# Performance work log

Hardware: AMD Instinct MI355X
Metric: run time of the kernel (lower is better)

The kernel has to match this reference:

```python
import jax, jax.numpy as jnp
import numpy as np

N = 40000      # nodes
E = 640000     # edges
R = 4          # relations (n_edge_features)
F = 128        # n_node_features
H = 128        # n_hidden
NB = 2         # num_convolution_blocks
G = 64         # graphs in batch
OUT = 10       # n_output
MAXDEG = 10    # PyG MFConv default max_degree


def setup_inputs() -> dict:
    key = jax.random.key(0)
    ks = jax.random.split(key, 20)
    s = 0.05
    return {
        "x": jax.random.normal(ks[0], (N, F), dtype=jnp.float32),
        "edge_index": jax.random.randint(ks[1], (2, E), 0, N, dtype=jnp.int32),
        "edge_attr": jax.random.randint(ks[2], (E,), 0, R, dtype=jnp.int32),
        "batch_idx": jnp.sort(jax.random.randint(ks[3], (N,), 0, G, dtype=jnp.int32)),
        # node embedding Linear(F -> H)
        "W0": jax.random.normal(ks[4], (F, H), dtype=jnp.float32) * s,
        "b0": jnp.zeros((H,), dtype=jnp.float32),
        # per-block RGCNConv params (stacked over blocks)
        "rgcn_Wrel": jax.random.normal(ks[5], (NB, R, H, H), dtype=jnp.float32) * s,
        "rgcn_Wroot": jax.random.normal(ks[6], (NB, H, H), dtype=jnp.float32) * s,
        "rgcn_b": jnp.zeros((NB, H), dtype=jnp.float32),
        # per-block MFConv params: lins_l (bias) and lins_r (no bias), one per degree 0..MAXDEG
        "mf_Wl": jax.random.normal(ks[7], (NB, MAXDEG + 1, H, H), dtype=jnp.float32) * s,
        "mf_bl": jnp.zeros((NB, MAXDEG + 1, H), dtype=jnp.float32),
        "mf_Wr": jax.random.normal(ks[8], (NB, MAXDEG + 1, H, H), dtype=jnp.float32) * s,
        # after-pool MLP
        "W1": jax.random.normal(ks[9], (H, H), dtype=jnp.float32) * s,
        "b1": jnp.zeros((H,), dtype=jnp.float32),
        "W2": jax.random.normal(ks[10], (H, OUT), dtype=jnp.float32) * s,
        "b2": jnp.zeros((OUT,), dtype=jnp.float32),
    }


def _rgcn(h, Wrel, Wroot, b, src, dst, etype):
    # PyG RGCNConv: per-relation mean of neighbor features, then relation GEMM, plus root + bias
    n = h.shape[0]
    idx = dst * R + etype                                   # fused (node, relation) segment id
    msg = h[src]                                            # [E, H] gather
    sums = jax.ops.segment_sum(msg, idx, num_segments=n * R).reshape(n, R, -1)
    cnt = jax.ops.segment_sum(jnp.ones((msg.shape[0],), h.dtype), idx,
                              num_segments=n * R).reshape(n, R, 1)
    mean = jnp.where(cnt > 0, sums / jnp.maximum(cnt, 1.0), 0.0)
    return jnp.einsum('nrh,rho->no', mean, Wrel) + h @ Wroot + b


def _mfconv(h, Wl, bl, Wr, src, dst, deg):
    # PyG MFConv: sum-aggregate neighbors, then degree-specific lin_l(agg) + lin_r(x)
    n = h.shape[0]
    agg = jax.ops.segment_sum(h[src], dst, num_segments=n)  # [N, H]
    out = jnp.zeros((n, Wl.shape[-1]), h.dtype)
    for d in range(MAXDEG + 1):                             # small fixed loop over degree buckets
        m = (deg == d).astype(h.dtype)[:, None]
        out = out + m * (agg @ Wl[d] + bl[d] + h @ Wr[d])
    return out


def reference(x, edge_index, edge_attr, batch_idx,
              W0, b0, rgcn_Wrel, rgcn_Wroot, rgcn_b,
              mf_Wl, mf_bl, mf_Wr, W1, b1, W2, b2):
    src, dst = edge_index[0], edge_index[1]
    etype = edge_attr
    n = x.shape[0]
    # node degree at targets (all relations), clamped to MAXDEG (PyG MFConv)
    deg = jnp.clip(jax.ops.segment_sum(jnp.ones((src.shape[0],), jnp.int32), dst,
                                       num_segments=n), 0, MAXDEG)
    h = x @ W0 + b0
    for blk in range(NB):
        h = jax.nn.relu(h)
        h = _rgcn(h, rgcn_Wrel[blk], rgcn_Wroot[blk], rgcn_b[blk], src, dst, etype)
        h = jax.nn.relu(h)
        h = _mfconv(h, mf_Wl[blk], mf_bl[blk], mf_Wr[blk], src, dst, deg)
    pooled = jax.ops.segment_sum(h, batch_idx, num_segments=G)  # global add pool [G, H]
    out = jax.nn.relu(pooled @ W1 + b1) @ W2 + b2
    return out
```

## Files before the change

kernel.cpp:

```cpp
#include <hip/hip_runtime.h>
#include <hip/hip_bf16.h>

#define N_NODES 40000
#define N_EDGES 640000
#define R_REL 4
#define F_IN 128
#define H_DIM 128
#define NBLK 2
#define G_GRAPHS 64
#define N_OUT 10
#define MAXDEG 10
#define NSCAN_BLK ((N_NODES + 255) / 256)

typedef unsigned short u16;
typedef float f32x4 __attribute__((ext_vector_type(4)));
typedef short bf16x8 __attribute__((ext_vector_type(8)));

__device__ __forceinline__ float relu_f(float x){ return x > 0.f ? x : 0.f; }

__device__ __forceinline__ u16 f2bf(float f){
  union { float f; unsigned int u; } v; v.f = f;
  unsigned int r = v.u + 0x7fffu + ((v.u >> 16) & 1u);
  return (u16)(r >> 16);
}
__device__ __forceinline__ float b2f(u16 u){
  union { unsigned int u; float f; } v; v.u = ((unsigned int)u) << 16; return v.f;
}
__device__ __forceinline__ float blo(unsigned v){ return b2f((u16)v); }
__device__ __forceinline__ float bhi(unsigned v){ return b2f((u16)(v >> 16)); }

__device__ __forceinline__ void gload16(const void* g, void* l){
  __builtin_amdgcn_global_load_lds(
      (const __attribute__((address_space(1))) void*)g,
      (__attribute__((address_space(3))) void*)l, 16, 0, 0);
}

__device__ __forceinline__ void unpk8(uint4 v, float* f){
  f[0] = blo(v.x); f[1] = bhi(v.x);
  f[2] = blo(v.y); f[3] = bhi(v.y);
  f[4] = blo(v.z); f[5] = bhi(v.z);
  f[6] = blo(v.w); f[7] = bhi(v.w);
}

__global__ void k_cnt(const int* __restrict__ dst, const int* __restrict__ et, int* __restrict__ cnt4){
  int e = blockIdx.x * blockDim.x + threadIdx.x;
  if (e >= N_EDGES) return;
  atomicAdd(&cnt4[dst[e] * R_REL + et[e]], 1);
}

__global__ __launch_bounds__(256) void k_scan_a(const int* __restrict__ cnt4, int* __restrict__ deg,
                                                int* __restrict__ row_ptr, int* __restrict__ bsum,
                                                int* __restrict__ bhist){
  __shared__ int s[256];
  __shared__ int lh[16];
  int tid = threadIdx.x;
  int i = blockIdx.x * 256 + tid;
  if (tid < 16) lh[tid] = 0;
  int d = 0;
  if (i < N_NODES){
    int4 c = *(const int4*)(cnt4 + (size_t)i * 4);
    d = c.x + c.y + c.z + c.w;
    deg[i] = d;
  }
  s[tid] = d;
  __syncthreads();
  if (i < N_NODES){
    int dc = d > MAXDEG ? MAXDEG : d;
    atomicAdd(&lh[dc], 1);
  }
  for (int o = 1; o < 256; o <<= 1){
    int t = (tid >= o) ? s[tid - o] : 0;
    __syncthreads();
    s[tid] += t;
    __syncthreads();
  }
  if (i < N_NODES) row_ptr[i] = s[tid] - d;
  if (tid == 255) bsum[blockIdx.x] = s[255];
  if (tid <= MAXDEG) bhist[blockIdx.x * (MAXDEG + 1) + tid] = lh[tid];
}

__global__ __launch_bounds__(256) void k_scan_bb(int* __restrict__ bsum, int* __restrict__ bbase,
                                                 const int* __restrict__ bhist, int* __restrict__ pbase,
                                                 int* __restrict__ bcount, int* __restrict__ boff){
  __shared__ int s[256];
  __shared__ int cnt_s[MAXDEG + 1];
  __shared__ int off_s[MAXDEG + 1];
  int tid = threadIdx.x;
  int v = (tid < NSCAN_BLK) ? bsum[tid] : 0;
  s[tid] = v;
  __syncthreads();
  for (int o = 1; o < 256; o <<= 1){
    int t = (tid >= o) ? s[tid - o] : 0;
    __syncthreads();
    s[tid] += t;
    __syncthreads();
  }
  if (tid < NSCAN_BLK) bbase[tid] = s[tid] - v;

  if (tid <= MAXDEG){
    int run = 0;
    for (int b = 0; b < NSCAN_BLK; ++b){
      pbase[b * (MAXDEG + 1) + tid] = run;
      run += bhist[b * (MAXDEG + 1) + tid];
    }
    cnt_s[tid] = run;
    bcount[tid] = run;
  }
  __syncthreads();
  if (tid == 0){
    int acc = 0;
    for (int dd = 0; dd <= MAXDEG; ++dd){ off_s[dd] = acc; boff[dd] = acc; acc += cnt_s[dd]; }
  }
  __syncthreads();
  if (tid <= MAXDEG){
    int base = off_s[tid];
    for (int b = 0; b < NSCAN_BLK; ++b) pbase[b * (MAXDEG + 1) + tid] += base;
  }
}

__global__ __launch_bounds__(256) void k_scan_c(int* __restrict__ row_ptr, const int* __restrict__ bbase,
                                                const int* __restrict__ cnt4, int* __restrict__ rel_off,
                                                int* __restrict__ cursor){
  int i = blockIdx.x * 256 + threadIdx.x;
  if (i < N_NODES){
    int base = row_ptr[i] + bbase[blockIdx.x];
    row_ptr[i] = base;
    int4 c = *(const int4*)(cnt4 + (size_t)i * 4);
    int4 o;
    o.x = base;
    o.y = base + c.x;
    o.z = o.y + c.y;
    o.w = o.z + c.z;
    *(int4*)(rel_off + (size_t)i * 4) = o;
    *(int4*)(cursor + (size_t)i * 4) = o;
  }
  if (i == 0) row_ptr[N_NODES] = N_EDGES;
}

__global__ void k_csr_fill(const int* __restrict__ src, const int* __restrict__ dst,
                           const int* __restrict__ et,
                           int* __restrict__ cursor, int* __restrict__ esrc){
  int e = blockIdx.x * blockDim.x + threadIdx.x;
  if (e >= N_EDGES) return;
  int cell = dst[e] * R_REL + et[e];
  int p = atomicAdd(&cursor[cell], 1);
  esrc[p] = src[e];
}

__global__ __launch_bounds__(256) void k_bfill_goff(const int* __restrict__ deg, const int* __restrict__ pbase,
                                                    int* __restrict__ perm,
                                                    const int* __restrict__ batch, int* __restrict__ goff){
  __shared__ int lh[MAXDEG + 1];
  int tid = threadIdx.x;
  if (tid <= MAXDEG) lh[tid] = 0;
  __syncthreads();
  int i = blockIdx.x * 256 + tid;
  if (i < N_NODES){
    int d = deg[i]; if (d > MAXDEG) d = MAXDEG;
    int lpos = atomicAdd(&lh[d], 1);
    perm[pbase[blockIdx.x * (MAXDEG + 1) + d] + lpos] = i;

    int b = batch[i];
    int bp = (i == 0) ? -1 : batch[i - 1];
    for (int g = bp + 1; g <= b; ++g) goff[g] = i;
    if (i == N_NODES - 1){
      for (int g = b + 1; g <= G_GRAPHS; ++g) goff[g] = N_NODES;
    }
  }
}

__global__ __launch_bounds__(256) void k_cvtW_all(const float* __restrict__ s0, const float* __restrict__ s1,
                                                  const float* __restrict__ s2, const float* __restrict__ s3,
                                                  const float* __restrict__ s4,
                                                  u16* __restrict__ d0, u16* __restrict__ d1,
                                                  u16* __restrict__ d2, u16* __restrict__ d3,
                                                  u16* __restrict__ d4){
  __shared__ float s[32][33];
  int b = blockIdx.x;
  int m = b >> 4, tile = b & 15;
  const float* S; u16* D; int base;
  if (m < 1){ S = s0; D = d0; base = m; }
  else if (m < 9){ S = s1; D = d1; base = m - 1; }
  else if (m < 11){ S = s2; D = d2; base = m - 9; }
  else if (m < 33){ S = s3; D = d3; base = m - 11; }
  else { S = s4; D = d4; base = m - 33; }
  S += (size_t)base * 16384;
  D += (size_t)base * 16384;
  int tr = (tile >> 2) * 32, tc = (tile & 3) * 32;
  int c = threadIdx.x & 31, r0 = threadIdx.x >> 5;
  #pragma unroll
  for (int i = 0; i < 4; ++i){
    int r = r0 + i * 8;
    s[r][c] = S[(size_t)(tr + r) * 128 + tc + c];
  }
  __syncthreads();
  #pragma unroll
  for (int i = 0; i < 4; ++i){
    int r = r0 + i * 8;
    D[(size_t)(tc + r) * 128 + tr + c] = f2bf(s[c][r]);
  }
}

__global__ __launch_bounds__(256) void k_rgcn_agg(const u16* __restrict__ hb,
                                                  const int* __restrict__ rel_off,
                                                  const int* __restrict__ row_ptr,
                                                  const int* __restrict__ esrc,
                                                  u16* __restrict__ meanb){
  int node = blockIdx.x * 4 + (threadIdx.x >> 6);
  int lane = threadIdx.x & 63;
  int g = lane >> 4, c = lane & 15;
  int gbase = lane & 48;
  int4 ro = *(const int4*)(rel_off + (size_t)node * 4);
  int nend = row_ptr[node + 1];
  int beg_g = (g == 0) ? ro.x : (g == 1) ? ro.y : (g == 2) ? ro.z : ro.w;
  int end_g = (g == 0) ? ro.y : (g == 1) ? ro.z : (g == 2) ? ro.w : nend;
  int cnt = end_g - beg_g;
  int spre = (c < cnt) ? esrc[beg_g + c] : 0;
  int n16 = cnt < 16 ? cnt : 16;
  float acc[8];
  #pragma unroll
  for (int j = 0; j < 8; ++j) acc[j] = 0.f;
  const u16* hc = hb + c * 8;

  int e = 0;
  for (; e + 4 <= n16; e += 4){
    int s0 = __shfl(spre, gbase + e, 64);
    int s1 = __shfl(spre, gbase + e + 1, 64);
    int s2 = __shfl(spre, gbase + e + 2, 64);
    int s3 = __shfl(spre, gbase + e + 3, 64);
    uint4 v0 = *(const uint4*)(hc + (size_t)s0 * H_DIM);
    uint4 v1 = *(const uint4*)(hc + (size_t)s1 * H_DIM);
    uint4 v2 = *(const uint4*)(hc + (size_t)s2 * H_DIM);
    uint4 v3 = *(const uint4*)(hc + (size_t)s3 * H_DIM);
    float f0[8], f1[8], f2[8], f3[8];
    unpk8(v0, f0); unpk8(v1, f1); unpk8(v2, f2); unpk8(v3, f3);
    #pragma unroll
    for (int j = 0; j < 8; ++j) acc[j] += (f0[j] + f1[j]) + (f2[j] + f3[j]);
  }
  for (; e < n16; ++e){
    int s = __shfl(spre, gbase + e, 64);
    uint4 v = *(const uint4*)(hc + (size_t)s * H_DIM);
    float f[8];
    unpk8(v, f);
    #pragma unroll
    for (int j = 0; j < 8; ++j) acc[j] += f[j];
  }
  for (; e < cnt; ++e){
    int s = esrc[beg_g + e];
    uint4 v = *(const uint4*)(hc + (size_t)s * H_DIM);
    float f[8];
    unpk8(v, f);
    #pragma unroll
    for (int j = 0; j < 8; ++j) acc[j] += f[j];
  }
  float inv = cnt > 0 ? 1.f / (float)cnt : 0.f;
  unsigned p[4];
  #pragma unroll
  for (int q = 0; q < 4; ++q)
    p[q] = (unsigned)f2bf(acc[q * 2] * inv) | ((unsigned)f2bf(acc[q * 2 + 1] * inv) << 16);
  *(uint4*)(meanb + (size_t)node * R_REL * H_DIM + g * H_DIM + c * 8) =
      make_uint4(p[0], p[1], p[2], p[3]);
}

__global__ __launch_bounds__(256) void k_mf_agg(const u16* __restrict__ hb,
                                                const int* __restrict__ row_ptr,
                                                const int* __restrict__ esrc,
                                                u16* __restrict__ aggb){
  int node = blockIdx.x * 4 + (threadIdx.x >> 6);
  int lane = threadIdx.x & 63;
  int g = lane >> 4, c = lane & 15;
  int beg = row_ptr[node], end = row_ptr[node + 1];
  int T = end - beg;
  int spre = (lane < T) ? esrc[beg + lane] : 0;
  int n64 = T < 64 ? T : 64;
  float acc[8];
  #pragma unroll
  for (int j = 0; j < 8; ++j) acc[j] = 0.f;
  const u16* hc = hb + c * 8;

  int i = 0;
  for (; i + 8 <= n64; i += 8){
    int sA = __shfl(spre, i + g, 64);
    int sB = __shfl(spre, i + 4 + g, 64);
    uint4 vA = *(const uint4*)(hc + (size_t)sA * H_DIM);
    uint4 vB = *(const uint4*)(hc + (size_t)sB * H_DIM);
    float fA[8], fB[8];
    unpk8(vA, fA); unpk8(vB, fB);
    #pragma unroll
    for (int j = 0; j < 8; ++j) acc[j] += fA[j] + fB[j];
  }
  for (; i < n64; i += 4){
    int e = i + g;
    int ce = e < n64 ? e : n64 - 1;
    int s = __shfl(spre, ce, 64);
    uint4 v = *(const uint4*)(hc + (size_t)s * H_DIM);
    float f[8];
    unpk8(v, f);
    float m = (e < n64) ? 1.f : 0.f;
    #pragma unroll
    for (int j = 0; j < 8; ++j) acc[j] += f[j] * m;
  }
  for (int e2 = 64 + g; e2 < T; e2 += 4){
    int s = esrc[beg + e2];
    uint4 v = *(const uint4*)(hc + (size_t)s * H_DIM);
    float f[8];
    unpk8(v, f);
    #pragma unroll
    for (int j = 0; j < 8; ++j) acc[j] += f[j];
  }
  #pragma unroll
  for (int j = 0; j < 8; ++j){
    acc[j] += __shfl_xor(acc[j], 16, 64);
    acc[j] += __shfl_xor(acc[j], 32, 64);
  }
  if (g == 0){
    unsigned p[4];
    #pragma unroll
    for (int q = 0; q < 4; ++q)
      p[q] = (unsigned)f2bf(acc[q * 2]) | ((unsigned)f2bf(acc[q * 2 + 1]) << 16);
    uint4 P = make_uint4(p[0], p[1], p[2], p[3]);
    *(uint4*)(aggb + (size_t)node * H_DIM + c * 8) = P;
  }
}


__global__ __launch_bounds__(512) void k_gemm0(const float* __restrict__ x, const u16* __restrict__ wt,
                                               const float* __restrict__ bias, u16* __restrict__ hbo){
  __shared__ u16 lds[32][128];
  int tid = threadIdx.x;
  int w = tid >> 6, lane = tid & 63;
  int m0 = blockIdx.x * 32;
  {
    int rg = lane >> 4, cb = (lane & 15) << 4;
    int srow = w * 4 + rg;
    int swcb = cb ^ ((srow & 7) << 4);
    const float* xs = x + (size_t)(m0 + srow) * F_IN + (swcb >> 1);
    float4 u = *(const float4*)xs;
    float4 v = *(const float4*)(xs + 4);
    unsigned p0 = (unsigned)f2bf(u.x) | ((unsigned)f2bf(u.y) << 16);
    unsigned p1 = (unsigned)f2bf(u.z) | ((unsigned)f2bf(u.w) << 16);
    unsigned p2 = (unsigned)f2bf(v.x) | ((unsigned)f2bf(v.y) << 16);
    unsigned p3 = (unsigned)f2bf(v.z) | ((unsigned)f2bf(v.w) << 16);
    *(uint4*)((char*)&lds[0][0] + w * 1024 + lane * 16) = make_uint4(p0, p1, p2, p3);
  }
  __syncthreads();

  int arow = lane & 15, kg = lane >> 4;
  int col = w * 16 + arow;
  f32x4 acc[2];
  acc[0] = (f32x4){0.f, 0.f, 0.f, 0.f};
  acc[1] = (f32x4){0.f, 0.f, 0.f, 0.f};
  bf16x8 b[4];
  #pragma unroll
  for (int kk = 0; kk < 4; ++kk)
    b[kk] = *(const bf16x8*)(wt + (size_t)col * F_IN + kk * 32 + kg * 8);
  #pragma unroll
  for (int rt = 0; rt < 2; ++rt){
    int row = rt * 16 + arow;
    const char* base = (const char*)&lds[0][0] + row * 256;
    int sx = (row & 7) << 4;
    #pragma unroll
    for (int kk = 0; kk < 4; ++kk){
      bf16x8 a = *(const bf16x8*)(base + ((kk * 64 + kg * 16) ^ sx));
      acc[rt] = __builtin_amdgcn_mfma_f32_16x16x32_bf16(a, b[kk], acc[rt], 0, 0, 0);
    }
  }
  float bb = bias[col];
  #pragma unroll
  for (int rt = 0; rt < 2; ++rt)
    #pragma unroll
    for (int j = 0; j < 4; ++j){
      int gr = m0 + rt * 16 + kg * 4 + j;
      hbo[(size_t)gr * H_DIM + col] = f2bf(relu_f(acc[rt][j] + bb));
    }
}

__global__ __launch_bounds__(512) void k_rgcn_gemm(const u16* __restrict__ meanb, const u16* __restrict__ hb,
                                                   const u16* __restrict__ wrel, const u16* __restrict__ wroot,
                                                   const float* __restrict__ bias, u16* __restrict__ hbo){
  __shared__ u16 lds[5][32][128];
  int tid = threadIdx.x;
  int w = tid >> 6, lane = tid & 63;
  int m0 = blockIdx.x * 32;
  int rg = lane >> 4, cb = (lane & 15) << 4;
  int srow = w * 4 + rg;
  int swcb = cb ^ ((srow & 7) << 4);
  #pragma unroll
  for (int s = 0; s < 4; ++s)
    gload16(meanb + ((size_t)(m0 + srow) * R_REL + s) * H_DIM + (swcb >> 1), &lds[s][w * 4][0]);
  gload16(hb + (size_t)(m0 + srow) * H_DIM + (swcb >> 1), &lds[4][w * 4][0]);
  __syncthreads();

  int arow = lane & 15, kg = lane >> 4;
  int col = w * 16 + arow;
  f32x4 acc[2];
  acc[0] = (f32x4){0.f, 0.f, 0.f, 0.f};
  acc[1] = (f32x4){0.f, 0.f, 0.f, 0.f};
  #pragma unroll
  for (int s = 0; s < 5; ++s){
    const u16* WT = (s < 4) ? wrel + (size_t)s * 16384 : wroot;
    bf16x8 b[4];
    #pragma unroll
    for (int kk = 0; kk < 4; ++kk)
      b[kk] = *(const bf16x8*)(WT + (size_t)col * H_DIM + kk * 32 + kg * 8);
    #pragma unroll
    for (int rt = 0; rt < 2; ++rt){
      int row = rt * 16 + arow;
      const char* base = (const char*)&lds[s][0][0] + row * 256;
      int sx = (row & 7) << 4;
      #pragma unroll
      for (int kk = 0; kk < 4; ++kk){
        bf16x8 a = *(const bf16x8*)(base + ((kk * 64 + kg * 16) ^ sx));
        acc[rt] = __builtin_amdgcn_mfma_f32_16x16x32_bf16(a, b[kk], acc[rt], 0, 0, 0);
      }
    }
  }
  float bb = bias[col];
  #pragma unroll
  for (int rt = 0; rt < 2; ++rt)
    #pragma unroll
    for (int j = 0; j < 4; ++j){
      int gr = m0 + rt * 16 + kg * 4 + j;
      hbo[(size_t)gr * H_DIM + col] = f2bf(relu_f(acc[rt][j] + bb));
    }
}

template<int FINAL>
__global__ __launch_bounds__(512) void k_mf_gemm(const u16* __restrict__ aggb, const u16* __restrict__ hb,
                                                 const u16* __restrict__ wl, const u16* __restrict__ wr,
                                                 const float* __restrict__ bl,
                                                 const int* __restrict__ bcount, const int* __restrict__ boff,
                                                 const int* __restrict__ perm,
                                                 u16* __restrict__ hbo, float* __restrict__ hf){
  __shared__ u16 lds[2][32][128];
  __shared__ int rows_s[32];
  int t = blockIdx.x;
  int d = -1, tile = 0;
  for (int dd = 0; dd <= MAXDEG; ++dd){
    int nt = (bcount[dd] + 31) >> 5;
    if (t < nt){ d = dd; tile = t; break; }
    t -= nt;
  }
  if (d < 0) return;
  int cnt_d = bcount[d];
  int start = boff[d] + tile * 32;
  int nrows = cnt_d - tile * 32; if (nrows > 32) nrows = 32;

  int tid = threadIdx.x;
  int w = tid >> 6, lane = tid & 63;
  if (tid < 32) rows_s[tid] = (tid < nrows) ? perm[start + tid] : -1;

  int rg = lane >> 4, cb = (lane & 15) << 4;
  int srow = w * 4 + rg;
  int swcb = cb ^ ((srow & 7) << 4);
  int node = perm[start + (srow < nrows ? srow : 0)];
  gload16(aggb + (size_t)node * H_DIM + (swcb >> 1), &lds[0][w * 4][0]);
  gload16(hb   + (size_t)node * H_DIM + (swcb >> 1), &lds[1][w * 4][0]);
  __syncthreads();

  int arow = lane & 15, kg = lane >> 4;
  int col = w * 16 + arow;
  f32x4 acc[2];
  acc[0] = (f32x4){0.f, 0.f, 0.f, 0.f};
  acc[1] = (f32x4){0.f, 0.f, 0.f, 0.f};
  #pragma unroll
  for (int s = 0; s < 2; ++s){
    const u16* WT = (s ? wr : wl) + (size_t)d * 16384;
    bf16x8 b[4];
    #pragma unroll
    for (int kk = 0; kk < 4; ++kk)
      b[kk] = *(const bf16x8*)(WT + (size_t)col * H_DIM + kk * 32 + kg * 8);
    #pragma unroll
    for (int rt = 0; rt < 2; ++rt){
      int row = rt * 16 + arow;
      const char* base = (const char*)&lds[s][0][0] + row * 256;
      int sx = (row & 7) << 4;
      #pragma unroll
      for (int kk = 0; kk < 4; ++kk){
        bf16x8 a = *(const bf16x8*)(base + ((kk * 64 + kg * 16) ^ sx));
        acc[rt] = __builtin_amdgcn_mfma_f32_16x16x32_bf16(a, b[kk], acc[rt], 0, 0, 0);
      }
    }
  }
  float bb = bl[(size_t)d * H_DIM + col];
  #pragma unroll
  for (int rt = 0; rt < 2; ++rt)
    #pragma unroll
    for (int j = 0; j < 4; ++j){
      int gr = rows_s[rt * 16 + kg * 4 + j];
      if (gr >= 0){
        float v = acc[rt][j] + bb;
        if (FINAL) hf[(size_t)gr * H_DIM + col] = v;
        else       hbo[(size_t)gr * H_DIM + col] = f2bf(relu_f(v));
      }
    }
}

__global__ __launch_bounds__(256) void k_poolmlp(const float* __restrict__ h, const int* __restrict__ goff,
                                                 const float* __restrict__ W1, const float* __restrict__ b1,
                                                 const float* __restrict__ W2, const float* __restrict__ b2,
                                                 float* __restrict__ out){
  __shared__ float4 sred[8][32];
  __shared__ float pv[128];
  __shared__ float Ts[128];
  int g = blockIdx.x;
  int tid = threadIdx.x;
  int rg = tid >> 5, lane = tid & 31;
  int beg = goff[g], end = goff[g + 1];
  float4 acc = make_float4(0.f, 0.f, 0.f, 0.f);
  for (int n = beg + rg; n < end; n += 8){
    float4 v = ((const float4*)(h + (size_t)n * H_DIM))[lane];
    acc.x += v.x; acc.y += v.y; acc.z += v.z; acc.w += v.w;
  }
  sred[rg][lane] = acc;
  __syncthreads();
  if (tid < 32){
    float4 s = sred[0][tid];
    #pragma unroll
    for (int r = 1; r < 8; ++r){
      float4 v = sred[r][tid];
      s.x += v.x; s.y += v.y; s.z += v.z; s.w += v.w;
    }
    *(float4*)&pv[tid * 4] = s;
  }
  __syncthreads();
  if (tid < 128){
    float s = b1[tid];
    for (int k = 0; k < H_DIM; ++k) s += pv[k] * W1[k * H_DIM + tid];
    Ts[tid] = relu_f(s);
  }
  __syncthreads();
  if (tid < N_OUT){
    float o = b2[tid];
    for (int k = 0; k < H_DIM; ++k) o += Ts[k] * W2[k * N_OUT + tid];
    out[(size_t)g * N_OUT + tid] = o;
  }
}

extern "C" void kernel_launch(void* const* d_in, const int* in_sizes, int n_in,
                              void* d_out, int out_size, void* d_ws, size_t ws_size,
                              hipStream_t stream){
  const float* x      = (const float*)d_in[0];
  const int*   ei     = (const int*)d_in[1];
  const int*   ea     = (const int*)d_in[2];
  const int*   batch  = (const int*)d_in[3];
  const float* W0     = (const float*)d_in[4];
  const float* b0     = (const float*)d_in[5];
  const float* rWrel  = (const float*)d_in[6];
  const float* rWroot = (const float*)d_in[7];
  const float* rb     = (const float*)d_in[8];
  const float* mWl    = (const float*)d_in[9];
  const float* mbl    = (const float*)d_in[10];
  const float* mWr    = (const float*)d_in[11];
  const float* W1     = (const float*)d_in[12];
  const float* b1     = (const float*)d_in[13];
  const float* W2     = (const float*)d_in[14];
  const float* b2     = (const float*)d_in[15];
  float* out = (float*)d_out;

  const int* src = ei;
  const int* dst = ei + N_EDGES;

  char* ws = (char*)d_ws;
  size_t off = 0;
  auto alloc = [&](size_t bytes) -> void* {
    void* p = ws + off;
    off += (bytes + 255) & ~(size_t)255;
    return p;
  };
  u16* hbA     = (u16*)alloc((size_t)N_NODES * H_DIM * 2);
  u16* hbB     = (u16*)alloc((size_t)N_NODES * H_DIM * 2);
  u16* meanb   = (u16*)alloc((size_t)N_NODES * R_REL * H_DIM * 2);
  u16* aggb    = meanb;
  float* hf    = (float*)alloc((size_t)N_NODES * H_DIM * 4);
  u16* wt0     = (u16*)alloc((size_t)1 * 16384 * 2);
  u16* wtRel   = (u16*)alloc((size_t)NBLK * R_REL * 16384 * 2);
  u16* wtRoot  = (u16*)alloc((size_t)NBLK * 16384 * 2);
  u16* wtWl    = (u16*)alloc((size_t)NBLK * (MAXDEG + 1) * 16384 * 2);
  u16* wtWr    = (u16*)alloc((size_t)NBLK * (MAXDEG + 1) * 16384 * 2);
  int* cnt4     = (int*)alloc((size_t)N_NODES * R_REL * 4);
  int* deg      = (int*)alloc((size_t)N_NODES * 4);
  int* row_ptr  = (int*)alloc((size_t)(N_NODES + 1) * 4);
  int* rel_off  = (int*)alloc((size_t)N_NODES * R_REL * 4);
  int* cursor   = (int*)alloc((size_t)N_NODES * R_REL * 4);
  int* esrc     = (int*)alloc((size_t)N_EDGES * 4);
  int* bsum     = (int*)alloc((size_t)NSCAN_BLK * 4);
  int* bbase    = (int*)alloc((size_t)NSCAN_BLK * 4);
  int* bhist    = (int*)alloc((size_t)NSCAN_BLK * (MAXDEG + 1) * 4);
  int* pbase    = (int*)alloc((size_t)NSCAN_BLK * (MAXDEG + 1) * 4);
  int* perm     = (int*)alloc((size_t)N_NODES * 4);
  int* bcount   = (int*)alloc(16 * 4);
  int* boff     = (int*)alloc(16 * 4);
  int* goff     = (int*)alloc((size_t)(G_GRAPHS + 1) * 4);

  hipMemsetAsync(cnt4, 0, (size_t)N_NODES * R_REL * 4, stream);

  k_cnt<<<(N_EDGES + 255) / 256, 256, 0, stream>>>(dst, ea, cnt4);
  k_scan_a<<<NSCAN_BLK, 256, 0, stream>>>(cnt4, deg, row_ptr, bsum, bhist);
  k_scan_bb<<<1, 256, 0, stream>>>(bsum, bbase, bhist, pbase, bcount, boff);
  k_scan_c<<<NSCAN_BLK, 256, 0, stream>>>(row_ptr, bbase, cnt4, rel_off, cursor);
  k_csr_fill<<<(N_EDGES + 255) / 256, 256, 0, stream>>>(src, dst, ea, cursor, esrc);
  k_bfill_goff<<<NSCAN_BLK, 256, 0, stream>>>(deg, pbase, perm, batch, goff);

  k_cvtW_all<<<55 * 16, 256, 0, stream>>>(W0, rWrel, rWroot, mWl, mWr,
                                          wt0, wtRel, wtRoot, wtWl, wtWr);

  k_gemm0<<<N_NODES / 32, 512, 0, stream>>>(x, wt0, b0, hbA);

  u16* hin = hbA;
  u16* hout = hbB;
  for (int blk = 0; blk < NBLK; ++blk){
    k_rgcn_agg<<<N_NODES / 4, 256, 0, stream>>>(hin, rel_off, row_ptr, esrc, meanb);
    k_rgcn_gemm<<<N_NODES / 32, 512, 0, stream>>>(meanb, hin,
        wtRel + (size_t)blk * R_REL * 16384,
        wtRoot + (size_t)blk * 16384,
        rb + (size_t)blk * H_DIM, hout);
    { u16* tmp = hin; hin = hout; hout = tmp; }

    k_mf_agg<<<N_NODES / 4, 256, 0, stream>>>(hin, row_ptr, esrc, aggb);
    const u16* wl_b = wtWl + (size_t)blk * (MAXDEG + 1) * 16384;
    const u16* wr_b = wtWr + (size_t)blk * (MAXDEG + 1) * 16384;
    const float* bl_b = mbl + (size_t)blk * (MAXDEG + 1) * H_DIM;
    int grid_mf = N_NODES / 32 + MAXDEG + 1;
    if (blk == NBLK - 1)
      k_mf_gemm<1><<<grid_mf, 512, 0, stream>>>(aggb, hin, wl_b, wr_b, bl_b,
                                                bcount, boff, perm, hout, hf);
    else
      k_mf_gemm<0><<<grid_mf, 512, 0, stream>>>(aggb, hin, wl_b, wr_b, bl_b,
                                                bcount, boff, perm, hout, hf);
    { u16* tmp = hin; hin = hout; hout = tmp; }
  }

  k_poolmlp<<<G_GRAPHS, 256, 0, stream>>>(hf, goff, W1, b1, W2, b2, out);
}
```

Before: 341.7 us.

## Fuse graph preprocessing and weight conversion into one cooperative kernel

Merges the memset, degree count, three-phase scan, CSR fill, bucket permutation, graph offsets and weight bf16 conversion into a single cooperative kernel that separates phases with grid-wide syncs. The aim is to remove seven kernel launches and their inter-kernel gaps. In exchange the edge-parallel atomic phases now run on only 157 blocks with grid-stride loops, so they get less parallelism, and each grid sync has its own cost.

```diff
diff --git a/kernel.cpp b/kernel.cpp
--- a/kernel.cpp
+++ b/kernel.cpp
@@ -1,5 +1,8 @@
 #include <hip/hip_runtime.h>
 #include <hip/hip_bf16.h>
+#include <hip/hip_cooperative_groups.h>
+
+namespace cg = cooperative_groups;
 
 #define N_NODES 40000
 #define N_EDGES 640000
@@ -42,162 +45,164 @@
   f[6] = blo(v.w); f[7] = bhi(v.w);
 }
 
-__global__ void k_cnt(const int* __restrict__ dst, const int* __restrict__ et, int* __restrict__ cnt4){
-  int e = blockIdx.x * blockDim.x + threadIdx.x;
-  if (e >= N_EDGES) return;
-  atomicAdd(&cnt4[dst[e] * R_REL + et[e]], 1);
-}
-
-__global__ __launch_bounds__(256) void k_scan_a(const int* __restrict__ cnt4, int* __restrict__ deg,
-                                                int* __restrict__ row_ptr, int* __restrict__ bsum,
-                                                int* __restrict__ bhist){
+__global__ __launch_bounds__(256) void k_setup(
+    const int* __restrict__ src, const int* __restrict__ dst, const int* __restrict__ et,
+    const int* __restrict__ batch,
+    const float* __restrict__ W0, const float* __restrict__ rWrel, const float* __restrict__ rWroot,
+    const float* __restrict__ mWl, const float* __restrict__ mWr,
+    u16* __restrict__ wt0, u16* __restrict__ wtRel, u16* __restrict__ wtRoot,
+    u16* __restrict__ wtWl, u16* __restrict__ wtWr,
+    int* __restrict__ cnt4, int* __restrict__ deg, int* __restrict__ row_ptr,
+    int* __restrict__ bsum, int* __restrict__ bhist, int* __restrict__ bbase,
+    int* __restrict__ pbase, int* __restrict__ bcount, int* __restrict__ boff,
+    int* __restrict__ rel_off, int* __restrict__ cursor, int* __restrict__ esrc,
+    int* __restrict__ perm, int* __restrict__ goff)
+{
+  cg::grid_group grid = cg::this_grid();
+  __shared__ float sw[32][33];
   __shared__ int s[256];
   __shared__ int lh[16];
+
   int tid = threadIdx.x;
-  int i = blockIdx.x * 256 + tid;
-  if (tid < 16) lh[tid] = 0;
-  int d = 0;
-  if (i < N_NODES){
-    int4 c = *(const int4*)(cnt4 + (size_t)i * 4);
-    d = c.x + c.y + c.z + c.w;
-    deg[i] = d;
-  }
-  s[tid] = d;
-  __syncthreads();
-  if (i < N_NODES){
-    int dc = d > MAXDEG ? MAXDEG : d;
-    atomicAdd(&lh[dc], 1);
-  }
-  for (int o = 1; o < 256; o <<= 1){
-    int t = (tid >= o) ? s[tid - o] : 0;
+  int bid = blockIdx.x;
+  int gtid = bid * 256 + tid;
+  int gsz = gridDim.x * 256;
+
+  for (int i = gtid; i < N_NODES * R_REL; i += gsz) cnt4[i] = 0;
+  grid.sync();
+
+  for (int e = gtid; e < N_EDGES; e += gsz)
+    atomicAdd(&cnt4[dst[e] * R_REL + et[e]], 1);
+
+  for (int b = bid; b < 55 * 16; b += gridDim.x){
+    int m = b >> 4, tile = b & 15;
+    const float* S; u16* D; int base;
+    if (m < 1){ S = W0; D = wt0; base = m; }
+    else if (m < 9){ S = rWrel; D = wtRel; base = m - 1; }
+    else if (m < 11){ S = rWroot; D = wtRoot; base = m - 9; }
+    else if (m < 33){ S = mWl; D = wtWl; base = m - 11; }
+    else { S = mWr; D = wtWr; base = m - 33; }
+    S += (size_t)base * 16384;
+    D += (size_t)base * 16384;
+    int tr = (tile >> 2) * 32, tc = (tile & 3) * 32;
+    int c = tid & 31, r0 = tid >> 5;
+    #pragma unroll
+    for (int i = 0; i < 4; ++i){
+      int r = r0 + i * 8;
+      sw[r][c] = S[(size_t)(tr + r) * 128 + tc + c];
+    }
     __syncthreads();
-    s[tid] += t;
+    #pragma unroll
+    for (int i = 0; i < 4; ++i){
+      int r = r0 + i * 8;
+      D[(size_t)(tc + r) * 128 + tr + c] = f2bf(sw[c][r]);
+    }
     __syncthreads();
   }
-  if (i < N_NODES) row_ptr[i] = s[tid] - d;
-  if (tid == 255) bsum[blockIdx.x] = s[255];
-  if (tid <= MAXDEG) bhist[blockIdx.x * (MAXDEG + 1) + tid] = lh[tid];
-}
-
-__global__ __launch_bounds__(256) void k_scan_bb(int* __restrict__ bsum, int* __restrict__ bbase,
-                                                 const int* __restrict__ bhist, int* __restrict__ pbase,
-                                                 int* __restrict__ bcount, int* __restrict__ boff){
-  __shared__ int s[256];
-  __shared__ int cnt_s[MAXDEG + 1];
-  __shared__ int off_s[MAXDEG + 1];
-  int tid = threadIdx.x;
-  int v = (tid < NSCAN_BLK) ? bsum[tid] : 0;
-  s[tid] = v;
-  __syncthreads();
-  for (int o = 1; o < 256; o <<= 1){
-    int t = (tid >= o) ? s[tid - o] : 0;
+  grid.sync();
+
+  {
+    int i = bid * 256 + tid;
+    if (tid < 16) lh[tid] = 0;
+    int d = 0;
+    if (i < N_NODES){
+      int4 c = *(const int4*)(cnt4 + (size_t)i * 4);
+      d = c.x + c.y + c.z + c.w;
+      deg[i] = d;
+    }
+    s[tid] = d;
     __syncthreads();
-    s[tid] += t;
+    if (i < N_NODES){
+      int dc = d > MAXDEG ? MAXDEG : d;
+      atomicAdd(&lh[dc], 1);
+    }
+    for (int o = 1; o < 256; o <<= 1){
+      int t = (tid >= o) ? s[tid - o] : 0;
+      __syncthreads();
+      s[tid] += t;
+      __syncthreads();
+    }
+    if (i < N_NODES) row_ptr[i] = s[tid] - d;
+    if (tid == 255) bsum[bid] = s[255];
+    if (tid <= MAXDEG) bhist[bid * (MAXDEG + 1) + tid] = lh[tid];
+  }
+  grid.sync();
+
+  if (bid == 0){
+    __shared__ int cnt_s[MAXDEG + 1];
+    __shared__ int off_s[MAXDEG + 1];
+    int v = (tid < NSCAN_BLK) ? bsum[tid] : 0;
+    s[tid] = v;
     __syncthreads();
-  }
-  if (tid < NSCAN_BLK) bbase[tid] = s[tid] - v;
-
-  if (tid <= MAXDEG){
-    int run = 0;
-    for (int b = 0; b < NSCAN_BLK; ++b){
-      pbase[b * (MAXDEG + 1) + tid] = run;
-      run += bhist[b * (MAXDEG + 1) + tid];
-    }
-    cnt_s[tid] = run;
-    bcount[tid] = run;
-  }
-  __syncthreads();
-  if (tid == 0){
-    int acc = 0;
-    for (int dd = 0; dd <= MAXDEG; ++dd){ off_s[dd] = acc; boff[dd] = acc; acc += cnt_s[dd]; }
-  }
-  __syncthreads();
-  if (tid <= MAXDEG){
-    int base = off_s[tid];
-    for (int b = 0; b < NSCAN_BLK; ++b) pbase[b * (MAXDEG + 1) + tid] += base;
-  }
-}
-
-__global__ __launch_bounds__(256) void k_scan_c(int* __restrict__ row_ptr, const int* __restrict__ bbase,
-                                                const int* __restrict__ cnt4, int* __restrict__ rel_off,
-                                                int* __restrict__ cursor){
-  int i = blockIdx.x * 256 + threadIdx.x;
-  if (i < N_NODES){
-    int base = row_ptr[i] + bbase[blockIdx.x];
-    row_ptr[i] = base;
-    int4 c = *(const int4*)(cnt4 + (size_t)i * 4);
-    int4 o;
-    o.x = base;
-    o.y = base + c.x;
-    o.z = o.y + c.y;
-    o.w = o.z + c.z;
-    *(int4*)(rel_off + (size_t)i * 4) = o;
-    *(int4*)(cursor + (size_t)i * 4) = o;
-  }
-  if (i == 0) row_ptr[N_NODES] = N_EDGES;
-}
-
-__global__ void k_csr_fill(const int* __restrict__ src, const int* __restrict__ dst,
-                           const int* __restrict__ et,
-                           int* __restrict__ cursor, int* __restrict__ esrc){
-  int e = blockIdx.x * blockDim.x + threadIdx.x;
-  if (e >= N_EDGES) return;
-  int cell = dst[e] * R_REL + et[e];
-  int p = atomicAdd(&cursor[cell], 1);
-  esrc[p] = src[e];
-}
-
-__global__ __launch_bounds__(256) void k_bfill_goff(const int* __restrict__ deg, const int* __restrict__ pbase,
-                                                    int* __restrict__ perm,
-                                                    const int* __restrict__ batch, int* __restrict__ goff){
-  __shared__ int lh[MAXDEG + 1];
-  int tid = threadIdx.x;
-  if (tid <= MAXDEG) lh[tid] = 0;
-  __syncthreads();
-  int i = blockIdx.x * 256 + tid;
-  if (i < N_NODES){
-    int d = deg[i]; if (d > MAXDEG) d = MAXDEG;
-    int lpos = atomicAdd(&lh[d], 1);
-    perm[pbase[blockIdx.x * (MAXDEG + 1) + d] + lpos] = i;
-
-    int b = batch[i];
-    int bp = (i == 0) ? -1 : batch[i - 1];
-    for (int g = bp + 1; g <= b; ++g) goff[g] = i;
-    if (i == N_NODES - 1){
-      for (int g = b + 1; g <= G_GRAPHS; ++g) goff[g] = N_NODES;
-    }
-  }
-}
-
-__global__ __launch_bounds__(256) void k_cvtW_all(const float* __restrict__ s0, const float* __restrict__ s1,
-                                                  const float* __restrict__ s2, const float* __restrict__ s3,
-                                                  const float* __restrict__ s4,
-                                                  u16* __restrict__ d0, u16* __restrict__ d1,
-                                                  u16* __restrict__ d2, u16* __restrict__ d3,
-                                                  u16* __restrict__ d4){
-  __shared__ float s[32][33];
-  int b = blockIdx.x;
-  int m = b >> 4, tile = b & 15;
-  const float* S; u16* D; int base;
-  if (m < 1){ S = s0; D = d0; base = m; }
-  else if (m < 9){ S = s1; D = d1; base = m - 1; }
-  else if (m < 11){ S = s2; D = d2; base = m - 9; }
-  else if (m < 33){ S = s3; D = d3; base = m - 11; }
-  else { S = s4; D = d4; base = m - 33; }
-  S += (size_t)base * 16384;
-  D += (size_t)base * 16384;
-  int tr = (tile >> 2) * 32, tc = (tile & 3) * 32;
-  int c = threadIdx.x & 31, r0 = threadIdx.x >> 5;
-  #pragma unroll
-  for (int i = 0; i < 4; ++i){
-    int r = r0 + i * 8;
-    s[r][c] = S[(size_t)(tr + r) * 128 + tc + c];
-  }
-  __syncthreads();
-  #pragma unroll
-  for (int i = 0; i < 4; ++i){
-    int r = r0 + i * 8;
-    D[(size_t)(tc + r) * 128 + tr + c] = f2bf(s[c][r]);
+    for (int o = 1; o < 256; o <<= 1){
+      int t = (tid >= o) ? s[tid - o] : 0;
+      __syncthreads();
+      s[tid] += t;
+      __syncthreads();
+    }
+    if (tid < NSCAN_BLK) bbase[tid] = s[tid] - v;
+
+    if (tid <= MAXDEG){
+      int run = 0;
+      for (int b = 0; b < NSCAN_BLK; ++b){
+        pbase[b * (MAXDEG + 1) + tid] = run;
+        run += bhist[b * (MAXDEG + 1) + tid];
+      }
+      cnt_s[tid] = run;
+      bcount[tid] = run;
+    }
+    __syncthreads();
+    if (tid == 0){
+      int acc = 0;
+      for (int dd = 0; dd <= MAXDEG; ++dd){ off_s[dd] = acc; boff[dd] = acc; acc += cnt_s[dd]; }
+    }
+    __syncthreads();
+    if (tid <= MAXDEG){
+      int base = off_s[tid];
+      for (int b = 0; b < NSCAN_BLK; ++b) pbase[b * (MAXDEG + 1) + tid] += base;
+    }
+  }
+  grid.sync();
+
+  {
+    int i = bid * 256 + tid;
+    if (i < N_NODES){
+      int base = row_ptr[i] + bbase[bid];
+      row_ptr[i] = base;
+      int4 c = *(const int4*)(cnt4 + (size_t)i * 4);
+      int4 o;
+      o.x = base;
+      o.y = base + c.x;
+      o.z = o.y + c.y;
+      o.w = o.z + c.z;
+      *(int4*)(rel_off + (size_t)i * 4) = o;
+      *(int4*)(cursor + (size_t)i * 4) = o;
+    }
+    if (i == 0) row_ptr[N_NODES] = N_EDGES;
+  }
+  grid.sync();
+
+  for (int e = gtid; e < N_EDGES; e += gsz){
+    int cell = dst[e] * R_REL + et[e];
+    int p = atomicAdd(&cursor[cell], 1);
+    esrc[p] = src[e];
+  }
+  {
+    if (tid <= MAXDEG) lh[tid] = 0;
+    __syncthreads();
+    int i = bid * 256 + tid;
+    if (i < N_NODES){
+      int d = deg[i]; if (d > MAXDEG) d = MAXDEG;
+      int lpos = atomicAdd(&lh[d], 1);
+      perm[pbase[bid * (MAXDEG + 1) + d] + lpos] = i;
+
+      int b = batch[i];
+      int bp = (i == 0) ? -1 : batch[i - 1];
+      for (int g = bp + 1; g <= b; ++g) goff[g] = i;
+      if (i == N_NODES - 1){
+        for (int g = b + 1; g <= G_GRAPHS; ++g) goff[g] = N_NODES;
+      }
+    }
   }
 }
 
@@ -593,17 +598,17 @@
   int* boff     = (int*)alloc(16 * 4);
   int* goff     = (int*)alloc((size_t)(G_GRAPHS + 1) * 4);
 
-  hipMemsetAsync(cnt4, 0, (size_t)N_NODES * R_REL * 4, stream);
-
-  k_cnt<<<(N_EDGES + 255) / 256, 256, 0, stream>>>(dst, ea, cnt4);
-  k_scan_a<<<NSCAN_BLK, 256, 0, stream>>>(cnt4, deg, row_ptr, bsum, bhist);
-  k_scan_bb<<<1, 256, 0, stream>>>(bsum, bbase, bhist, pbase, bcount, boff);
-  k_scan_c<<<NSCAN_BLK, 256, 0, stream>>>(row_ptr, bbase, cnt4, rel_off, cursor);
-  k_csr_fill<<<(N_EDGES + 255) / 256, 256, 0, stream>>>(src, dst, ea, cursor, esrc);
-  k_bfill_goff<<<NSCAN_BLK, 256, 0, stream>>>(deg, pbase, perm, batch, goff);
-
-  k_cvtW_all<<<55 * 16, 256, 0, stream>>>(W0, rWrel, rWroot, mWl, mWr,
-                                          wt0, wtRel, wtRoot, wtWl, wtWr);
+  {
+    void* args[] = {
+      (void*)&src, (void*)&dst, (void*)&ea, (void*)&batch,
+      (void*)&W0, (void*)&rWrel, (void*)&rWroot, (void*)&mWl, (void*)&mWr,
+      (void*)&wt0, (void*)&wtRel, (void*)&wtRoot, (void*)&wtWl, (void*)&wtWr,
+      (void*)&cnt4, (void*)&deg, (void*)&row_ptr, (void*)&bsum, (void*)&bhist,
+      (void*)&bbase, (void*)&pbase, (void*)&bcount, (void*)&boff,
+      (void*)&rel_off, (void*)&cursor, (void*)&esrc, (void*)&perm, (void*)&goff
+    };
+    hipLaunchCooperativeKernel((void*)k_setup, dim3(NSCAN_BLK), dim3(256), args, 0, stream);
+  }
 
   k_gemm0<<<N_NODES / 32, 512, 0, stream>>>(x, wt0, b0, hbA);
 
```

Result: slower. 423.8 us (+24.0%).
